# Kernel tuning notes

Measured on AMD Instinct MI355X. Metric: run time of the kernel, lower is better.

The kernel has to match this reference:

```python
import jax, jax.numpy as jnp
import numpy as np


def _sage_layer(x, src, dst, W_self, W_neigh, b, n_nodes):
    # mean aggregation over incoming edges: agg[v] = mean(x[u] for (u,v) in E)
    agg = jax.ops.segment_sum(x[src], dst, num_segments=n_nodes)          # [N, D]
    cnt = jax.ops.segment_sum(jnp.ones((src.shape[0],), x.dtype), dst,
                              num_segments=n_nodes)                        # [N]
    agg = agg / jnp.clip(cnt, 1.0)[:, None]
    # h = ReLU(x W_self^T + agg W_neigh^T + b)   (torch Linear weight is [out, in])
    h = jnp.einsum('nd,od->no', x, W_self) + jnp.einsum('nd,od->no', agg, W_neigh) + b
    return jax.nn.relu(h)


def setup_inputs() -> dict:
    key = jax.random.key(0)
    ks = jax.random.split(key, 7)
    N, E = 50000, 800000
    F_IN, H, F_OUT = 128, 256, 128
    x = jax.random.normal(ks[0], (N, F_IN), dtype=jnp.float32)
    edge_index = jax.random.randint(ks[1], (2, E), 0, N, dtype=jnp.int64)
    s = 0.05
    return {
        'x': x,
        'edge_index': edge_index,
        'W_self1': jax.random.normal(ks[2], (H, F_IN), dtype=jnp.float32) * s,
        'W_neigh1': jax.random.normal(ks[3], (H, F_IN), dtype=jnp.float32) * s,
        'b1': jnp.zeros((H,), dtype=jnp.float32),
        'W_self2': jax.random.normal(ks[4], (F_OUT, H), dtype=jnp.float32) * s,
        'W_neigh2': jax.random.normal(ks[5], (F_OUT, H), dtype=jnp.float32) * s,
        'b2': jnp.zeros((F_OUT,), dtype=jnp.float32),
    }


def reference(x, edge_index, W_self1, W_neigh1, b1, W_self2, W_neigh2, b2):
    n_nodes = x.shape[0]
    src, dst = edge_index[0], edge_index[1]
    h = _sage_layer(x, src, dst, W_self1, W_neigh1, b1, n_nodes)
    # dropout is identity at inference
    h = _sage_layer(h, src, dst, W_self2, W_neigh2, b2, n_nodes)
    return h
```

## Files before the change

kernel.cpp:

```cpp
#include <hip/hip_runtime.h>


#define CAP 64
#define CPAD 16
#define NSLICE 8

typedef __attribute__((ext_vector_type(8))) short bfrag;
typedef __attribute__((ext_vector_type(4))) float ffrag;

__device__ inline unsigned short f2bf(float f) {
    union { float f; unsigned u; } v; v.f = f;
    unsigned r = (v.u + 0x7FFFu + ((v.u >> 16) & 1u)) >> 16;
    return (unsigned short)r;
}

__global__ __launch_bounds__(256) void prep_kernel(
        const int* __restrict__ src, const int* __restrict__ dst,
        int* __restrict__ cnt, unsigned short* __restrict__ adj,
        int E, int nper, int nfill,
        const float* __restrict__ x, unsigned short* __restrict__ xb, long xn4,
        int xblocks,
        const float* __restrict__ W0, const float* __restrict__ W1,
        const float* __restrict__ W2, const float* __restrict__ W3,
        unsigned short* __restrict__ O0, unsigned short* __restrict__ O1,
        unsigned short* __restrict__ O2, unsigned short* __restrict__ O3)
{
    int b = blockIdx.x;
    if (b < nfill) {
        int slice = b & (NSLICE - 1);
        int e = (b >> 3) * 256 + (int)threadIdx.x;
        if (e >= E) return;
        int d = __builtin_nontemporal_load(dst + e);
        if ((unsigned)(d - slice * nper) >= (unsigned)nper) return;
        int s = __builtin_nontemporal_load(src + e);
        int r = atomicAdd(&cnt[d * CPAD], 1);
        if (r < CAP) adj[(size_t)d * CAP + r] = (unsigned short)s;
        return;
    }
    b -= nfill;
    if (b < xblocks) {
        long i = (long)b * 256 + threadIdx.x;
        if (i >= xn4) return;
        float4 v = *(const float4*)(x + i * 4);
        ushort4 o;
        o.x = f2bf(v.x); o.y = f2bf(v.y); o.z = f2bf(v.z); o.w = f2bf(v.w);
        *(ushort4*)(xb + i * 4) = o;
        return;
    }
    b -= xblocks;
    int i = b * 256 + (int)threadIdx.x;
    int sel = i >> 13, off = i & 8191;
    const float* srcw = (sel == 0) ? W0 : (sel == 1) ? W1 : (sel == 2) ? W2 : W3;
    unsigned short* dstw = (sel == 0) ? O0 : (sel == 1) ? O1 : (sel == 2) ? O2 : O3;
    float4 v = ((const float4*)srcw)[off];
    ushort4 o;
    o.x = f2bf(v.x); o.y = f2bf(v.y); o.z = f2bf(v.z); o.w = f2bf(v.w);
    ((ushort4*)dstw)[off] = o;
}

#define BFLO(u) __uint_as_float((u) << 16)
#define BFHI(u) __uint_as_float((u) & 0xFFFF0000u)

#define ACC8(V)  do {                                                          \
    acc0 += BFLO(V.x); acc1 += BFHI(V.x); acc2 += BFLO(V.y); acc3 += BFHI(V.y);\
    acc4 += BFLO(V.z); acc5 += BFHI(V.z); acc6 += BFLO(V.w); acc7 += BFHI(V.w);\
} while (0)

__global__ __launch_bounds__(256) void gather_mean_bf16(
        const unsigned short* __restrict__ Xb, const int* __restrict__ cnt,
        const unsigned short* __restrict__ adj,
        unsigned short* __restrict__ aggb, int N) {
    int w = (blockIdx.x * 256 + threadIdx.x) >> 6;
    int lane = threadIdx.x & 63;
    int node = w * 4 + (lane >> 4);
    int sl = lane & 15;
    if (node >= N) return;
    int c = cnt[node * CPAD]; if (c > CAP) c = CAP;
    const unsigned short* al = adj + (size_t)node * CAP;
    float acc0 = 0.f, acc1 = 0.f, acc2 = 0.f, acc3 = 0.f;
    float acc4 = 0.f, acc5 = 0.f, acc6 = 0.f, acc7 = 0.f;
    int j = 0;
    for (; j + 3 < c; j += 4) {
        ushort4 q = *(const ushort4*)(al + j);
        uint4 v0 = *(const uint4*)(Xb + (size_t)q.x * 128 + sl * 8);
        uint4 v1 = *(const uint4*)(Xb + (size_t)q.y * 128 + sl * 8);
        uint4 v2 = *(const uint4*)(Xb + (size_t)q.z * 128 + sl * 8);
        uint4 v3 = *(const uint4*)(Xb + (size_t)q.w * 128 + sl * 8);
        ACC8(v0); ACC8(v1); ACC8(v2); ACC8(v3);
    }
    for (; j < c; ++j) {
        uint4 v = *(const uint4*)(Xb + (size_t)al[j] * 128 + sl * 8);
        ACC8(v);
    }
    float s = (c > 0) ? 1.0f / (float)c : 0.0f;
    uint4 o;
    o.x = (unsigned)f2bf(acc0 * s) | ((unsigned)f2bf(acc1 * s) << 16);
    o.y = (unsigned)f2bf(acc2 * s) | ((unsigned)f2bf(acc3 * s) << 16);
    o.z = (unsigned)f2bf(acc4 * s) | ((unsigned)f2bf(acc5 * s) << 16);
    o.w = (unsigned)f2bf(acc6 * s) | ((unsigned)f2bf(acc7 * s) << 16);
    *(uint4*)(aggb + (size_t)node * 128 + sl * 8) = o;
}

__global__ __launch_bounds__(256) void gather_epilogue_bf16(
        const unsigned short* __restrict__ Zb, const unsigned short* __restrict__ S2b,
        const int* __restrict__ cnt, const unsigned short* __restrict__ adj,
        float* __restrict__ out, int N) {
    int w = (blockIdx.x * 256 + threadIdx.x) >> 6;
    int lane = threadIdx.x & 63;
    int node = w * 4 + (lane >> 4);
    int sl = lane & 15;
    if (node >= N) return;
    int c = cnt[node * CPAD]; if (c > CAP) c = CAP;
    const unsigned short* al = adj + (size_t)node * CAP;
    float acc0 = 0.f, acc1 = 0.f, acc2 = 0.f, acc3 = 0.f;
    float acc4 = 0.f, acc5 = 0.f, acc6 = 0.f, acc7 = 0.f;
    int j = 0;
    for (; j + 3 < c; j += 4) {
        ushort4 q = *(const ushort4*)(al + j);
        uint4 v0 = *(const uint4*)(Zb + (size_t)q.x * 128 + sl * 8);
        uint4 v1 = *(const uint4*)(Zb + (size_t)q.y * 128 + sl * 8);
        uint4 v2 = *(const uint4*)(Zb + (size_t)q.z * 128 + sl * 8);
        uint4 v3 = *(const uint4*)(Zb + (size_t)q.w * 128 + sl * 8);
        ACC8(v0); ACC8(v1); ACC8(v2); ACC8(v3);
    }
    for (; j < c; ++j) {
        uint4 v = *(const uint4*)(Zb + (size_t)al[j] * 128 + sl * 8);
        ACC8(v);
    }
    float s = (c > 0) ? 1.0f / (float)c : 0.0f;
    uint4 sv = *(const uint4*)(S2b + (size_t)node * 128 + sl * 8);
    float4 oa, ob;
    oa.x = fmaxf(BFLO(sv.x) + acc0 * s, 0.0f);
    oa.y = fmaxf(BFHI(sv.x) + acc1 * s, 0.0f);
    oa.z = fmaxf(BFLO(sv.y) + acc2 * s, 0.0f);
    oa.w = fmaxf(BFHI(sv.y) + acc3 * s, 0.0f);
    ob.x = fmaxf(BFLO(sv.z) + acc4 * s, 0.0f);
    ob.y = fmaxf(BFHI(sv.z) + acc5 * s, 0.0f);
    ob.z = fmaxf(BFLO(sv.w) + acc6 * s, 0.0f);
    ob.w = fmaxf(BFHI(sv.w) + acc7 * s, 0.0f);
    float* op = out + (size_t)node * 128 + sl * 8;
    *(float4*)op = oa;
    *(float4*)(op + 4) = ob;
}

#define L1_LOAD(NF, NTV) do {                                                  \
    const short* xr_ = xb   + (size_t)((NTV) * 16 + ln) * 128 + lk * 8;        \
    const short* ar_ = aggb + (size_t)((NTV) * 16 + ln) * 128 + lk * 8;        \
    _Pragma("unroll") for (int kc = 0; kc < 4; ++kc) {                         \
        NF[kc]     = *(const bfrag*)(xr_ + kc * 32);                           \
        NF[4 + kc] = *(const bfrag*)(ar_ + kc * 32); }                         \
} while (0)

#define L1_STEP(NF, CURNT) do {                                                \
    const int node_ = (CURNT) * 16 + ln;                                       \
    ffrag acc_[4];                                                             \
    _Pragma("unroll") for (int m = 0; m < 4; ++m) {                            \
        acc_[m][0] = bv[m].x; acc_[m][1] = bv[m].y;                            \
        acc_[m][2] = bv[m].z; acc_[m][3] = bv[m].w; }                          \
    _Pragma("unroll") for (int m = 0; m < 4; ++m) {                            \
        _Pragma("unroll") for (int kc = 0; kc < 4; ++kc)                       \
            acc_[m] = __builtin_amdgcn_mfma_f32_16x16x32_bf16(                 \
                wfs[m][kc], NF[kc], acc_[m], 0, 0, 0);                         \
        _Pragma("unroll") for (int kc = 0; kc < 4; ++kc)                       \
            acc_[m] = __builtin_amdgcn_mfma_f32_16x16x32_bf16(                 \
                wfn[m][kc], NF[4 + kc], acc_[m], 0, 0, 0); }                   \
    _Pragma("unroll") for (int m = 0; m < 4; ++m) {                            \
        ushort4 o_;                                                            \
        o_.x = f2bf(fmaxf(acc_[m][0], 0.f)); o_.y = f2bf(fmaxf(acc_[m][1], 0.f)); \
        o_.z = f2bf(fmaxf(acc_[m][2], 0.f)); o_.w = f2bf(fmaxf(acc_[m][3], 0.f)); \
        *(ushort4*)(h1b + (size_t)node_ * 256 + (wave * 4 + m) * 16 + lk * 4) = o_; } \
} while (0)

__global__ __launch_bounds__(256) void mfma_layer1(
        const short* __restrict__ xb, const short* __restrict__ aggb,
        const short* __restrict__ Ws, const short* __restrict__ Wn,
        const float* __restrict__ bias, unsigned short* __restrict__ h1b, int NT)
{
    const int wave = threadIdx.x >> 6, lane = threadIdx.x & 63;
    const int ln = lane & 15, lk = lane >> 4;

    bfrag wfs[4][4], wfn[4][4];
    #pragma unroll
    for (int m = 0; m < 4; ++m) {
        const short* ws = Ws + (size_t)((wave * 4 + m) * 16 + ln) * 128 + lk * 8;
        const short* wn = Wn + (size_t)((wave * 4 + m) * 16 + ln) * 128 + lk * 8;
        #pragma unroll
        for (int kc = 0; kc < 4; ++kc) {
            wfs[m][kc] = *(const bfrag*)(ws + kc * 32);
            wfn[m][kc] = *(const bfrag*)(wn + kc * 32);
        }
    }
    float4 bv[4];
    #pragma unroll
    for (int m = 0; m < 4; ++m)
        bv[m] = *(const float4*)(bias + (wave * 4 + m) * 16 + lk * 4);

    bfrag nfA[8], nfB[8];
    const int stride = gridDim.x;
    int nt = blockIdx.x;
    if (nt >= NT) return;
    L1_LOAD(nfA, nt);
    while (true) {
        int ntn = nt + stride;
        if (ntn < NT) L1_LOAD(nfB, ntn);
        L1_STEP(nfA, nt);
        nt = ntn; if (nt >= NT) break;
        ntn = nt + stride;
        if (ntn < NT) L1_LOAD(nfA, ntn);
        L1_STEP(nfB, nt);
        nt = ntn; if (nt >= NT) break;
    }
}

#define L2_LOAD(NF, NTV) do {                                                  \
    const short* hr_ = h1b + (size_t)((NTV) * 16 + ln) * 256 + lk * 8;         \
    _Pragma("unroll") for (int kc = 0; kc < 8; ++kc)                           \
        NF[kc] = *(const bfrag*)(hr_ + kc * 32);                               \
} while (0)

#define L2_STEP(NF, CURNT) do {                                                \
    const int node_ = (CURNT) * 16 + ln;                                       \
    ffrag aS_[2], aZ_[2];                                                      \
    _Pragma("unroll") for (int m = 0; m < 2; ++m) {                            \
        aS_[m][0] = bv[m].x; aS_[m][1] = bv[m].y;                              \
        aS_[m][2] = bv[m].z; aS_[m][3] = bv[m].w;                              \
        aZ_[m][0] = 0.f; aZ_[m][1] = 0.f; aZ_[m][2] = 0.f; aZ_[m][3] = 0.f; }  \
    _Pragma("unroll") for (int m = 0; m < 2; ++m)                              \
        _Pragma("unroll") for (int kc = 0; kc < 8; ++kc) {                     \
            aS_[m] = __builtin_amdgcn_mfma_f32_16x16x32_bf16(                  \
                wfs[m][kc], NF[kc], aS_[m], 0, 0, 0);                          \
            aZ_[m] = __builtin_amdgcn_mfma_f32_16x16x32_bf16(                  \
                wfn[m][kc], NF[kc], aZ_[m], 0, 0, 0); }                        \
    _Pragma("unroll") for (int m = 0; m < 2; ++m) {                            \
        ushort4 so_;                                                           \
        so_.x = f2bf(aS_[m][0]); so_.y = f2bf(aS_[m][1]);                      \
        so_.z = f2bf(aS_[m][2]); so_.w = f2bf(aS_[m][3]);                      \
        *(ushort4*)(s2b + (size_t)node_ * 128 + (wave * 2 + m) * 16 + lk * 4) = so_; \
        ushort4 zo_;                                                           \
        zo_.x = f2bf(aZ_[m][0]); zo_.y = f2bf(aZ_[m][1]);                      \
        zo_.z = f2bf(aZ_[m][2]); zo_.w = f2bf(aZ_[m][3]);                      \
        *(ushort4*)(z2b + (size_t)node_ * 128 + (wave * 2 + m) * 16 + lk * 4) = zo_; } \
} while (0)

__global__ __launch_bounds__(256) void mfma_layer2(
        const short* __restrict__ h1b, const short* __restrict__ Ws,
        const short* __restrict__ Wn, const float* __restrict__ bias,
        unsigned short* __restrict__ s2b, unsigned short* __restrict__ z2b, int NT)
{
    const int wave = threadIdx.x >> 6, lane = threadIdx.x & 63;
    const int ln = lane & 15, lk = lane >> 4;

    bfrag wfs[2][8], wfn[2][8];
    #pragma unroll
    for (int m = 0; m < 2; ++m) {
        const short* ws = Ws + (size_t)((wave * 2 + m) * 16 + ln) * 256 + lk * 8;
        const short* wn = Wn + (size_t)((wave * 2 + m) * 16 + ln) * 256 + lk * 8;
        #pragma unroll
        for (int kc = 0; kc < 8; ++kc) {
            wfs[m][kc] = *(const bfrag*)(ws + kc * 32);
            wfn[m][kc] = *(const bfrag*)(wn + kc * 32);
        }
    }
    float4 bv[2];
    #pragma unroll
    for (int m = 0; m < 2; ++m)
        bv[m] = *(const float4*)(bias + (wave * 2 + m) * 16 + lk * 4);

    bfrag nfA[8], nfB[8];
    const int stride = gridDim.x;
    int nt = blockIdx.x;
    if (nt >= NT) return;
    L2_LOAD(nfA, nt);
    while (true) {
        int ntn = nt + stride;
        if (ntn < NT) L2_LOAD(nfB, ntn);
        L2_STEP(nfA, nt);
        nt = ntn; if (nt >= NT) break;
        ntn = nt + stride;
        if (ntn < NT) L2_LOAD(nfA, ntn);
        L2_STEP(nfB, nt);
        nt = ntn; if (nt >= NT) break;
    }
}

extern "C" void kernel_launch(void* const* d_in, const int* in_sizes, int n_in,
                              void* d_out, int out_size, void* d_ws, size_t ws_size,
                              hipStream_t stream) {
    const float* x   = (const float*)d_in[0];
    const int*   ei  = (const int*)d_in[1];
    const float* Ws1 = (const float*)d_in[2];
    const float* Wn1 = (const float*)d_in[3];
    const float* b1  = (const float*)d_in[4];
    const float* Ws2 = (const float*)d_in[5];
    const float* Wn2 = (const float*)d_in[6];
    const float* b2  = (const float*)d_in[7];
    float* out = (float*)d_out;

    const int N = in_sizes[0] / 128;
    const int E = in_sizes[1] / 2;
    const int NT = N / 16;
    const int* src = ei;
    const int* dst = ei + E;

    unsigned short* xb   = (unsigned short*)d_ws;
    unsigned short* h1b  = xb   + (size_t)N * 128;
    unsigned short* aggb = h1b  + (size_t)N * 256;
    unsigned short* z2b  = aggb + (size_t)N * 128;
    unsigned short* s2b  = z2b  + (size_t)N * 128;
    unsigned short* Wsb1 = s2b  + (size_t)N * 128;
    unsigned short* Wnb1 = Wsb1 + 32768;
    unsigned short* Wsb2 = Wnb1 + 32768;
    unsigned short* Wnb2 = Wsb2 + 32768;
    int* cnt = (int*)(Wnb2 + 32768);
    unsigned short* adj = (unsigned short*)(cnt + (size_t)N * CPAD);

    const int nper    = (N + NSLICE - 1) / NSLICE;
    const int nfill   = ((E + 255) / 256) * NSLICE;
    const long xn4    = (long)N * 128 / 4;
    const int xblocks = (int)((xn4 + 255) / 256);
    const int prep_blocks = nfill + xblocks + 128;

    hipMemsetAsync(cnt, 0, (size_t)N * CPAD * sizeof(int), stream);
    prep_kernel<<<prep_blocks, 256, 0, stream>>>(
        src, dst, cnt, adj, E, nper, nfill,
        x, xb, xn4, xblocks,
        Ws1, Wn1, Ws2, Wn2, Wsb1, Wnb1, Wsb2, Wnb2);

    const int gather_blocks = (N * 16 + 255) / 256;

    gather_mean_bf16<<<gather_blocks, 256, 0, stream>>>(xb, cnt, adj, aggb, N);
    mfma_layer1<<<512, 256, 0, stream>>>(
        (const short*)xb, (const short*)aggb, (const short*)Wsb1, (const short*)Wnb1,
        b1, h1b, NT);

    mfma_layer2<<<512, 256, 0, stream>>>(
        (const short*)h1b, (const short*)Wsb2, (const short*)Wnb2, b2, s2b, z2b, NT);
    gather_epilogue_bf16<<<gather_blocks, 256, 0, stream>>>(
        z2b, s2b, cnt, adj, out, N);
}
```

Measured before the change: 242.5 us.

## Fuse layer-1 neighbor gather into MFMA GEMM via shared-memory aggregate tile

Merges the layer-1 mean-aggregation gather kernel into the layer-1 MFMA kernel. Each block gathers a 16-node aggregate tile into LDS, syncs, then runs the GEMM, so the bf16 aggregate no longer round-trips through global memory and one launch is removed. In exchange the gather now runs inside a 512-block persistent grid with only 16 nodes per iteration, two barriers per tile and no prefetch double-buffering, so latency hiding may suffer. It also drops the nontemporal loads on the edge arrays in prep.

```diff
diff --git a/kernel.cpp b/kernel.cpp
--- a/kernel.cpp
+++ b/kernel.cpp
@@ -30,9 +30,9 @@
         int slice = b & (NSLICE - 1);
         int e = (b >> 3) * 256 + (int)threadIdx.x;
         if (e >= E) return;
-        int d = __builtin_nontemporal_load(dst + e);
+        int d = dst[e];
         if ((unsigned)(d - slice * nper) >= (unsigned)nper) return;
-        int s = __builtin_nontemporal_load(src + e);
+        int s = src[e];
         int r = atomicAdd(&cnt[d * CPAD], 1);
         if (r < CAP) adj[(size_t)d * CAP + r] = (unsigned short)s;
         return;
@@ -66,39 +66,104 @@
     acc4 += BFLO(V.z); acc5 += BFHI(V.z); acc6 += BFLO(V.w); acc7 += BFHI(V.w);\
 } while (0)
 
-__global__ __launch_bounds__(256) void gather_mean_bf16(
-        const unsigned short* __restrict__ Xb, const int* __restrict__ cnt,
+__global__ __launch_bounds__(256, 2) void fused_l1(
+        const unsigned short* __restrict__ xbu, const int* __restrict__ cnt,
         const unsigned short* __restrict__ adj,
-        unsigned short* __restrict__ aggb, int N) {
-    int w = (blockIdx.x * 256 + threadIdx.x) >> 6;
-    int lane = threadIdx.x & 63;
-    int node = w * 4 + (lane >> 4);
-    int sl = lane & 15;
-    if (node >= N) return;
-    int c = cnt[node * CPAD]; if (c > CAP) c = CAP;
-    const unsigned short* al = adj + (size_t)node * CAP;
-    float acc0 = 0.f, acc1 = 0.f, acc2 = 0.f, acc3 = 0.f;
-    float acc4 = 0.f, acc5 = 0.f, acc6 = 0.f, acc7 = 0.f;
-    int j = 0;
-    for (; j + 3 < c; j += 4) {
-        ushort4 q = *(const ushort4*)(al + j);
-        uint4 v0 = *(const uint4*)(Xb + (size_t)q.x * 128 + sl * 8);
-        uint4 v1 = *(const uint4*)(Xb + (size_t)q.y * 128 + sl * 8);
-        uint4 v2 = *(const uint4*)(Xb + (size_t)q.z * 128 + sl * 8);
-        uint4 v3 = *(const uint4*)(Xb + (size_t)q.w * 128 + sl * 8);
-        ACC8(v0); ACC8(v1); ACC8(v2); ACC8(v3);
-    }
-    for (; j < c; ++j) {
-        uint4 v = *(const uint4*)(Xb + (size_t)al[j] * 128 + sl * 8);
-        ACC8(v);
-    }
-    float s = (c > 0) ? 1.0f / (float)c : 0.0f;
-    uint4 o;
-    o.x = (unsigned)f2bf(acc0 * s) | ((unsigned)f2bf(acc1 * s) << 16);
-    o.y = (unsigned)f2bf(acc2 * s) | ((unsigned)f2bf(acc3 * s) << 16);
-    o.z = (unsigned)f2bf(acc4 * s) | ((unsigned)f2bf(acc5 * s) << 16);
-    o.w = (unsigned)f2bf(acc6 * s) | ((unsigned)f2bf(acc7 * s) << 16);
-    *(uint4*)(aggb + (size_t)node * 128 + sl * 8) = o;
+        const short* __restrict__ Ws, const short* __restrict__ Wn,
+        const float* __restrict__ bias, unsigned short* __restrict__ h1b, int NT)
+{
+    const short* xb = (const short*)xbu;
+    const int wave = threadIdx.x >> 6, lane = threadIdx.x & 63;
+    const int ln = lane & 15, lk = lane >> 4;
+    const int gn = threadIdx.x >> 4;
+    const int sp = threadIdx.x & 15;
+
+    __shared__ unsigned short aggT[16][136];
+
+    bfrag wfs[4][4], wfn[4][4];
+    #pragma unroll
+    for (int m = 0; m < 4; ++m) {
+        const short* ws = Ws + (size_t)((wave * 4 + m) * 16 + ln) * 128 + lk * 8;
+        const short* wn = Wn + (size_t)((wave * 4 + m) * 16 + ln) * 128 + lk * 8;
+        #pragma unroll
+        for (int kc = 0; kc < 4; ++kc) {
+            wfs[m][kc] = *(const bfrag*)(ws + kc * 32);
+            wfn[m][kc] = *(const bfrag*)(wn + kc * 32);
+        }
+    }
+    float4 bv[4];
+    #pragma unroll
+    for (int m = 0; m < 4; ++m)
+        bv[m] = *(const float4*)(bias + (wave * 4 + m) * 16 + lk * 4);
+
+    for (int nt = blockIdx.x; nt < NT; nt += gridDim.x) {
+        {
+            int node = nt * 16 + gn;
+            int c = cnt[node * CPAD]; if (c > CAP) c = CAP;
+            const unsigned short* al = adj + (size_t)node * CAP;
+            float acc0 = 0.f, acc1 = 0.f, acc2 = 0.f, acc3 = 0.f;
+            float acc4 = 0.f, acc5 = 0.f, acc6 = 0.f, acc7 = 0.f;
+            int j = 0;
+            for (; j + 3 < c; j += 4) {
+                ushort4 q = *(const ushort4*)(al + j);
+                uint4 v0 = *(const uint4*)(xbu + (size_t)q.x * 128 + sp * 8);
+                uint4 v1 = *(const uint4*)(xbu + (size_t)q.y * 128 + sp * 8);
+                uint4 v2 = *(const uint4*)(xbu + (size_t)q.z * 128 + sp * 8);
+                uint4 v3 = *(const uint4*)(xbu + (size_t)q.w * 128 + sp * 8);
+                ACC8(v0); ACC8(v1); ACC8(v2); ACC8(v3);
+            }
+            for (; j < c; ++j) {
+                uint4 v = *(const uint4*)(xbu + (size_t)al[j] * 128 + sp * 8);
+                ACC8(v);
+            }
+            float s = (c > 0) ? 1.0f / (float)c : 0.0f;
+            uint4 o;
+            o.x = (unsigned)f2bf(acc0 * s) | ((unsigned)f2bf(acc1 * s) << 16);
+            o.y = (unsigned)f2bf(acc2 * s) | ((unsigned)f2bf(acc3 * s) << 16);
+            o.z = (unsigned)f2bf(acc4 * s) | ((unsigned)f2bf(acc5 * s) << 16);
+            o.w = (unsigned)f2bf(acc6 * s) | ((unsigned)f2bf(acc7 * s) << 16);
+            *(uint4*)(&aggT[gn][sp * 8]) = o;
+        }
+        __syncthreads();
+
+        {
+            const int node = nt * 16 + ln;
+            bfrag nf[8];
+            const short* xr = xb + (size_t)node * 128 + lk * 8;
+            #pragma unroll
+            for (int kc = 0; kc < 4; ++kc) {
+                nf[kc]     = *(const bfrag*)(xr + kc * 32);
+                nf[4 + kc] = *(const bfrag*)(&aggT[ln][lk * 8 + kc * 32]);
+            }
+            ffrag acc[4];
+            #pragma unroll
+            for (int m = 0; m < 4; ++m) {
+                acc[m][0] = bv[m].x; acc[m][1] = bv[m].y;
+                acc[m][2] = bv[m].z; acc[m][3] = bv[m].w;
+            }
+            #pragma unroll
+            for (int m = 0; m < 4; ++m) {
+                #pragma unroll
+                for (int kc = 0; kc < 4; ++kc)
+                    acc[m] = __builtin_amdgcn_mfma_f32_16x16x32_bf16(
+                        wfs[m][kc], nf[kc], acc[m], 0, 0, 0);
+                #pragma unroll
+                for (int kc = 0; kc < 4; ++kc)
+                    acc[m] = __builtin_amdgcn_mfma_f32_16x16x32_bf16(
+                        wfn[m][kc], nf[4 + kc], acc[m], 0, 0, 0);
+            }
+            #pragma unroll
+            for (int m = 0; m < 4; ++m) {
+                ushort4 o;
+                o.x = f2bf(fmaxf(acc[m][0], 0.f));
+                o.y = f2bf(fmaxf(acc[m][1], 0.f));
+                o.z = f2bf(fmaxf(acc[m][2], 0.f));
+                o.w = f2bf(fmaxf(acc[m][3], 0.f));
+                *(ushort4*)(h1b + (size_t)node * 256 + (wave * 4 + m) * 16 + lk * 4) = o;
+            }
+        }
+        __syncthreads();
+    }
 }
 
 __global__ __launch_bounds__(256) void gather_epilogue_bf16(
@@ -141,75 +206,6 @@
     float* op = out + (size_t)node * 128 + sl * 8;
     *(float4*)op = oa;
     *(float4*)(op + 4) = ob;
-}
-
-#define L1_LOAD(NF, NTV) do {                                                  \
-    const short* xr_ = xb   + (size_t)((NTV) * 16 + ln) * 128 + lk * 8;        \
-    const short* ar_ = aggb + (size_t)((NTV) * 16 + ln) * 128 + lk * 8;        \
-    _Pragma("unroll") for (int kc = 0; kc < 4; ++kc) {                         \
-        NF[kc]     = *(const bfrag*)(xr_ + kc * 32);                           \
-        NF[4 + kc] = *(const bfrag*)(ar_ + kc * 32); }                         \
-} while (0)
-
-#define L1_STEP(NF, CURNT) do {                                                \
-    const int node_ = (CURNT) * 16 + ln;                                       \
-    ffrag acc_[4];                                                             \
-    _Pragma("unroll") for (int m = 0; m < 4; ++m) {                            \
-        acc_[m][0] = bv[m].x; acc_[m][1] = bv[m].y;                            \
-        acc_[m][2] = bv[m].z; acc_[m][3] = bv[m].w; }                          \
-    _Pragma("unroll") for (int m = 0; m < 4; ++m) {                            \
-        _Pragma("unroll") for (int kc = 0; kc < 4; ++kc)                       \
-            acc_[m] = __builtin_amdgcn_mfma_f32_16x16x32_bf16(                 \
-                wfs[m][kc], NF[kc], acc_[m], 0, 0, 0);                         \
-        _Pragma("unroll") for (int kc = 0; kc < 4; ++kc)                       \
-            acc_[m] = __builtin_amdgcn_mfma_f32_16x16x32_bf16(                 \
-                wfn[m][kc], NF[4 + kc], acc_[m], 0, 0, 0); }                   \
-    _Pragma("unroll") for (int m = 0; m < 4; ++m) {                            \
-        ushort4 o_;                                                            \
-        o_.x = f2bf(fmaxf(acc_[m][0], 0.f)); o_.y = f2bf(fmaxf(acc_[m][1], 0.f)); \
-        o_.z = f2bf(fmaxf(acc_[m][2], 0.f)); o_.w = f2bf(fmaxf(acc_[m][3], 0.f)); \
-        *(ushort4*)(h1b + (size_t)node_ * 256 + (wave * 4 + m) * 16 + lk * 4) = o_; } \
-} while (0)
-
-__global__ __launch_bounds__(256) void mfma_layer1(
-        const short* __restrict__ xb, const short* __restrict__ aggb,
-        const short* __restrict__ Ws, const short* __restrict__ Wn,
-        const float* __restrict__ bias, unsigned short* __restrict__ h1b, int NT)
-{
-    const int wave = threadIdx.x >> 6, lane = threadIdx.x & 63;
-    const int ln = lane & 15, lk = lane >> 4;
-
-    bfrag wfs[4][4], wfn[4][4];
-    #pragma unroll
-    for (int m = 0; m < 4; ++m) {
-        const short* ws = Ws + (size_t)((wave * 4 + m) * 16 + ln) * 128 + lk * 8;
-        const short* wn = Wn + (size_t)((wave * 4 + m) * 16 + ln) * 128 + lk * 8;
-        #pragma unroll
-        for (int kc = 0; kc < 4; ++kc) {
-            wfs[m][kc] = *(const bfrag*)(ws + kc * 32);
-            wfn[m][kc] = *(const bfrag*)(wn + kc * 32);
-        }
-    }
-    float4 bv[4];
-    #pragma unroll
-    for (int m = 0; m < 4; ++m)
-        bv[m] = *(const float4*)(bias + (wave * 4 + m) * 16 + lk * 4);
-
-    bfrag nfA[8], nfB[8];
-    const int stride = gridDim.x;
-    int nt = blockIdx.x;
-    if (nt >= NT) return;
-    L1_LOAD(nfA, nt);
-    while (true) {
-        int ntn = nt + stride;
-        if (ntn < NT) L1_LOAD(nfB, ntn);
-        L1_STEP(nfA, nt);
-        nt = ntn; if (nt >= NT) break;
-        ntn = nt + stride;
-        if (ntn < NT) L1_LOAD(nfA, ntn);
-        L1_STEP(nfB, nt);
-        nt = ntn; if (nt >= NT) break;
-    }
 }
 
 #define L2_LOAD(NF, NTV) do {                                                  \
@@ -304,8 +300,7 @@
 
     unsigned short* xb   = (unsigned short*)d_ws;
     unsigned short* h1b  = xb   + (size_t)N * 128;
-    unsigned short* aggb = h1b  + (size_t)N * 256;
-    unsigned short* z2b  = aggb + (size_t)N * 128;
+    unsigned short* z2b  = h1b  + (size_t)N * 256;
     unsigned short* s2b  = z2b  + (size_t)N * 128;
     unsigned short* Wsb1 = s2b  + (size_t)N * 128;
     unsigned short* Wnb1 = Wsb1 + 32768;
@@ -326,15 +321,11 @@
         x, xb, xn4, xblocks,
         Ws1, Wn1, Ws2, Wn2, Wsb1, Wnb1, Wsb2, Wnb2);
 
-    const int gather_blocks = (N * 16 + 255) / 256;
-
-    gather_mean_bf16<<<gather_blocks, 256, 0, stream>>>(xb, cnt, adj, aggb, N);
-    mfma_layer1<<<512, 256, 0, stream>>>(
-        (const short*)xb, (const short*)aggb, (const short*)Wsb1, (const short*)Wnb1,
-        b1, h1b, NT);
+    fused_l1<<<512, 256, 0, stream>>>(
+        xb, cnt, adj, (const short*)Wsb1, (const short*)Wnb1, b1, h1b, NT);
 
     mfma_layer2<<<512, 256, 0, stream>>>(
         (const short*)h1b, (const short*)Wsb2, (const short*)Wnb2, b2, s2b, z2b, NT);
-    gather_epilogue_bf16<<<gather_blocks, 256, 0, stream>>>(
+    gather_epilogue_bf16<<<(N * 16 + 255) / 256, 256, 0, stream>>>(
         z2b, s2b, cnt, adj, out, N);
 }
```

Result: no change. 242.2 us (-0.1%).
